# Optimization experiments

Hardware: AMD Instinct MI355X
Metric: run time of the kernel (lower is better)

## Reference

```python
import math
import jax, jax.numpy as jnp
import numpy as np

B, N, D = 4, 4096, 1024
H, DH = 16, 64  # D == H * DH


def setup_inputs() -> dict:
    key = jax.random.key(0)
    ks = jax.random.split(key, 7)
    s = 1.0 / math.sqrt(D)
    return {
        "tens": jax.random.normal(ks[0], (B, N, D), dtype=jnp.float32),
        "Wq": jax.random.normal(ks[1], (D, D), dtype=jnp.float32) * s,
        "bq": jax.random.normal(ks[2], (D,), dtype=jnp.float32) * 0.01,
        "Wk": jax.random.normal(ks[3], (D, D), dtype=jnp.float32) * s,
        "bk": jax.random.normal(ks[4], (D,), dtype=jnp.float32) * 0.01,
        "Wv": jax.random.normal(ks[5], (D, D), dtype=jnp.float32) * s,
        "bv": jax.random.normal(ks[6], (D,), dtype=jnp.float32) * 0.01,
    }


def reference(tens, Wq, bq, Wk, bk, Wv, bv):
    b, n, d = tens.shape
    # projections (torch Linear: x @ W^T + b)
    q = (tens @ Wq.T + bq).reshape(b, n, H, DH)  # [B,N,H,DH]
    k = (tens @ Wk.T + bk).reshape(b, n, H, DH)
    v = (tens @ Wv.T + bv).reshape(b, n, H, DH)
    scale = (1.0 / math.sqrt(DH)) / math.sqrt(n)
    # No softmax between QK^T and V => linear, reassociate as Q @ (K^T V)
    # to avoid the O(N^2) attention matrix; identical math.
    ktv = jnp.einsum("bnhd,bnhe->bhde", k, v)          # [B,H,DH,DH]
    out = jnp.einsum("bnhd,bhde->bnhe", q, ktv) * scale  # [B,N,H,DH]
    return out.reshape(b, n, d)
```

## Files before the change

### kernel.cpp

```cpp
#include <hip/hip_runtime.h>

typedef unsigned short ushort_t;
typedef __attribute__((ext_vector_type(8))) __bf16 bf16x8;
typedef __attribute__((ext_vector_type(8))) unsigned short ushort8;
typedef __attribute__((ext_vector_type(4))) float floatx4;

__device__ inline unsigned short f2bf(float f) {
  union { float f; unsigned u; } x; x.f = f;
  return (unsigned short)((x.u + 0x7FFFu + ((x.u >> 16) & 1u)) >> 16);
}

__global__ void cvt_f32_bf16(const float* __restrict__ in, ushort_t* __restrict__ out, int n) {
  int i = (blockIdx.x * blockDim.x + threadIdx.x) * 8;
  if (i >= n) return;
  const float4* p = (const float4*)(in + i);
  float4 a = p[0], b = p[1];
  ushort8 o;
  o[0] = f2bf(a.x); o[1] = f2bf(a.y); o[2] = f2bf(a.z); o[3] = f2bf(a.w);
  o[4] = f2bf(b.x); o[5] = f2bf(b.y); o[6] = f2bf(b.z); o[7] = f2bf(b.w);
  *(ushort8*)(out + i) = o;
}

__device__ inline void gload_lds16(const void* g, void* l) {
  __builtin_amdgcn_global_load_lds(
      (const __attribute__((address_space(1))) unsigned int*)g,
      (__attribute__((address_space(3))) unsigned int*)l, 16, 0, 0);
}

__device__ inline void store_out(float* p, float v) { *p = v; }
__device__ inline void store_out(ushort_t* p, float v) { *p = f2bf(v); }

template <typename OutT>
__global__ void gemm_bt(const ushort_t* __restrict__ A, const ushort_t* __restrict__ Bm,
                        const float* __restrict__ bias, OutT* __restrict__ C,
                        int M, int N, long sA_, long sB_, long sBias_, long sC_) {
  const int K = 1024;

  int gx = gridDim.x, gxy = gridDim.x * gridDim.y;
  int flat = blockIdx.x + gx * blockIdx.y + gxy * blockIdx.z;
  int total = gxy * gridDim.z;
  int per = total >> 3;
  int nf = (flat & 7) * per + (flat >> 3);
  int bz = nf / gxy; int rem = nf - bz * gxy;
  int by = rem / gx; int bx = rem - by * gx;

  A += (long)bz * sA_; Bm += (long)bz * sB_; bias += (long)bz * sBias_; C += (long)bz * sC_;

  __shared__ ushort_t sA[128 * 32];
  __shared__ ushort_t sB[128 * 32];

  int t = threadIdx.x;
  int w = t >> 6, l = t & 63;
  int wy = w >> 1, wx = w & 1;
  int quad = l >> 4, m16 = l & 15;
  int mBase = by * 128, nBase = bx * 128;

  int r = l >> 2, pb = l & 3;
  int swzS = (r ^ (r >> 2)) & 3;
  int sRow0 = w * 32 + r;
  int sCol = (pb ^ swzS) * 8;
  const ushort_t* gA0 = A + (long)(mBase + sRow0) * K + sCol;
  const ushort_t* gA1 = gA0 + 16 * K;
  const ushort_t* gB0 = Bm + (long)(nBase + sRow0) * K + sCol;
  const ushort_t* gB1 = gB0 + 16 * K;
  ushort_t* lA0 = sA + (w * 2) * 512;
  ushort_t* lA1 = lA0 + 512;
  ushort_t* lB0 = sB + (w * 2) * 512;
  ushort_t* lB1 = lB0 + 512;

  int swzR = (m16 ^ (m16 >> 2)) & 3;
  int aOff = (wy * 64 + m16) * 32 + (quad ^ swzR) * 8;
  int bOff = (wx * 64 + m16) * 32 + (quad ^ swzR) * 8;

  floatx4 acc[4][4] = {};

  for (int kt = 0; kt < K; kt += 32) {
    __syncthreads();
    gload_lds16(gA0 + kt, lA0);
    gload_lds16(gA1 + kt, lA1);
    gload_lds16(gB0 + kt, lB0);
    gload_lds16(gB1 + kt, lB1);
    __syncthreads();
    bf16x8 af[4], bfr[4];
#pragma unroll
    for (int i = 0; i < 4; ++i) af[i] = *(const bf16x8*)(sA + aOff + i * 16 * 32);
#pragma unroll
    for (int i = 0; i < 4; ++i) bfr[i] = *(const bf16x8*)(sB + bOff + i * 16 * 32);
#pragma unroll
    for (int mi = 0; mi < 4; ++mi)
#pragma unroll
      for (int ni = 0; ni < 4; ++ni)
        acc[mi][ni] = __builtin_amdgcn_mfma_f32_16x16x32_bf16(af[mi], bfr[ni], acc[mi][ni], 0, 0, 0);
  }

#pragma unroll
  for (int ni = 0; ni < 4; ++ni) {
    int n = nBase + wx * 64 + ni * 16 + m16;
    float bb = bias[n];
#pragma unroll
    for (int mi = 0; mi < 4; ++mi) {
      int m0 = mBase + wy * 64 + mi * 16 + quad * 4;
      floatx4 v = acc[mi][ni];
#pragma unroll
      for (int rr = 0; rr < 4; ++rr)
        store_out(&C[(long)(m0 + rr) * N + n], v[rr] + bb);
    }
  }
}

__global__ void ktv_mfma(const ushort_t* __restrict__ Kb, const ushort_t* __restrict__ Vb,
                         float* __restrict__ part) {
  int bh = blockIdx.x, sl = blockIdx.y;
  int b = bh >> 4, h = bh & 15;
  __shared__ ushort_t sKT[64 * 40];
  __shared__ ushort_t sVT[64 * 40];
  int t = threadIdx.x;
  int w = t >> 6, l = t & 63;
  int quad = l >> 4, m16 = l & 15;
  int nr = t & 31, d0 = (t >> 5) * 8;
  long base = ((long)(b * 4096 + sl * 512)) * 1024 + h * 64;
  floatx4 acc[4] = {};
  for (int nc = 0; nc < 512; nc += 32) {
    __syncthreads();
    ushort8 kv = *(const ushort8*)(Kb + base + (long)(nc + nr) * 1024 + d0);
    ushort8 vv = *(const ushort8*)(Vb + base + (long)(nc + nr) * 1024 + d0);
#pragma unroll
    for (int i = 0; i < 8; ++i) {
      sKT[(d0 + i) * 40 + nr] = kv[i];
      sVT[(d0 + i) * 40 + nr] = vv[i];
    }
    __syncthreads();
    bf16x8 af = *(const bf16x8*)(sKT + (w * 16 + m16) * 40 + quad * 8);
#pragma unroll
    for (int j = 0; j < 4; ++j) {
      bf16x8 bf = *(const bf16x8*)(sVT + (j * 16 + m16) * 40 + quad * 8);
      acc[j] = __builtin_amdgcn_mfma_f32_16x16x32_bf16(af, bf, acc[j], 0, 0, 0);
    }
  }
  float* p = part + ((long)(bh * 8 + sl)) * 4096;
#pragma unroll
  for (int j = 0; j < 4; ++j)
#pragma unroll
    for (int rr = 0; rr < 4; ++rr)
      p[(w * 16 + quad * 4 + rr) * 64 + j * 16 + m16] = acc[j][rr];
}

__global__ void ktv_reduce(const float* __restrict__ part, float* __restrict__ ktv) {
  int i = blockIdx.x * 256 + threadIdx.x;
  int bh = i >> 12, de = i & 4095;
  float s = 0.f;
#pragma unroll
  for (int sl = 0; sl < 8; ++sl) s += part[((long)(bh * 8 + sl)) * 4096 + de];
  ktv[i] = s;
}

__global__ void make_w2(const float* __restrict__ Wq, const float* __restrict__ bq,
                        const float* __restrict__ ktv, ushort_t* __restrict__ W2T,
                        float* __restrict__ bias2, float scale) {
  int bh = blockIdx.x, cq = blockIdx.y;
  int b = bh >> 4, h = bh & 15;
  __shared__ float sKTV[64 * 64];
  __shared__ float sW[64 * 64];
  int t = threadIdx.x;
  for (int i = t * 4; i < 4096; i += 1024)
    *(float4*)(sKTV + i) = *(const float4*)(ktv + (long)bh * 4096 + i);
  __syncthreads();
  if (cq == 0 && t < 64) {
    float s = 0.f;
    for (int d = 0; d < 64; ++d) s += bq[h * 64 + d] * sKTV[d * 64 + t];
    bias2[b * 1024 + h * 64 + t] = s * scale;
  }
  int e = t >> 2, c0 = (t & 3) * 16;
  for (int ct = cq * 256; ct < cq * 256 + 256; ct += 64) {
    __syncthreads();
    {
      int d = t >> 2, cc = (t & 3) * 16;
#pragma unroll
      for (int j = 0; j < 16; j += 4)
        *(float4*)(sW + d * 64 + cc + j) =
            *(const float4*)(Wq + (long)(h * 64 + d) * 1024 + ct + cc + j);
    }
    __syncthreads();
    float outv[16] = {};
    for (int d = 0; d < 64; ++d) {
      float kv = sKTV[d * 64 + e];
#pragma unroll
      for (int j = 0; j < 16; ++j) outv[j] += sW[d * 64 + c0 + j] * kv;
    }
    ushort8 o0, o1;
#pragma unroll
    for (int j = 0; j < 8; ++j) { o0[j] = f2bf(outv[j] * scale); o1[j] = f2bf(outv[8 + j] * scale); }
    ushort_t* dst = W2T + ((long)(b * 1024 + h * 64 + e)) * 1024 + ct + c0;
    *(ushort8*)dst = o0;
    *(ushort8*)(dst + 8) = o1;
  }
}

extern "C" void kernel_launch(void* const* d_in, const int* in_sizes, int n_in,
                              void* d_out, int out_size, void* d_ws, size_t ws_size,
                              hipStream_t stream) {
  (void)in_sizes; (void)n_in; (void)out_size; (void)ws_size;
  const float* tens = (const float*)d_in[0];
  const float* Wq = (const float*)d_in[1];
  const float* bq = (const float*)d_in[2];
  const float* Wk = (const float*)d_in[3];
  const float* bk = (const float*)d_in[4];
  const float* Wv = (const float*)d_in[5];
  const float* bv = (const float*)d_in[6];
  float* out = (float*)d_out;

  char* w = (char*)d_ws;
  ushort_t* Xbf  = (ushort_t*)(w);
  ushort_t* Kbf  = (ushort_t*)(w + 33554432);
  ushort_t* Vbf  = (ushort_t*)(w + 67108864);
  ushort_t* Wkbf = (ushort_t*)(w + 100663296);
  ushort_t* Wvbf = (ushort_t*)(w + 102760448);
  float*    part = (float*)(w + 104857600);
  float*    ktv  = (float*)(w + 113246208);
  ushort_t* W2T  = (ushort_t*)(w + 114294784);
  float*    bias2= (float*)(w + 122683392);

  const float scale = (1.0f / 8.0f) / 64.0f;

  hipLaunchKernelGGL(cvt_f32_bf16, dim3(8192), dim3(256), 0, stream, tens, Xbf, 16777216);
  hipLaunchKernelGGL(cvt_f32_bf16, dim3(512), dim3(256), 0, stream, Wk, Wkbf, 1048576);
  hipLaunchKernelGGL(cvt_f32_bf16, dim3(512), dim3(256), 0, stream, Wv, Wvbf, 1048576);

  hipLaunchKernelGGL((gemm_bt<ushort_t>), dim3(8, 128, 1), dim3(256), 0, stream,
                     Xbf, Wkbf, bk, Kbf, 16384, 1024, 0L, 0L, 0L, 0L);
  hipLaunchKernelGGL((gemm_bt<ushort_t>), dim3(8, 128, 1), dim3(256), 0, stream,
                     Xbf, Wvbf, bv, Vbf, 16384, 1024, 0L, 0L, 0L, 0L);

  hipLaunchKernelGGL(ktv_mfma, dim3(64, 8), dim3(256), 0, stream, Kbf, Vbf, part);
  hipLaunchKernelGGL(ktv_reduce, dim3(1024), dim3(256), 0, stream, part, ktv);
  hipLaunchKernelGGL(make_w2, dim3(64, 4), dim3(256), 0, stream, Wq, bq, ktv, W2T, bias2, scale);

  hipLaunchKernelGGL((gemm_bt<float>), dim3(8, 32, 4), dim3(256), 0, stream,
                     Xbf, W2T, bias2, out, 4096, 1024,
                     4194304L, 1048576L, 1024L, 4194304L);
}
```

Baseline: 316.2 us.

## Replace 128x128 GEMM with 256x256 tile, 4-stage LDS pipeline

Swaps the 128x128 single-buffered GEMM for a 256x256 tile kernel with 512 threads and a 4-deep LDS ring. It prefetches two tiles ahead with direct global-to-LDS loads and uses manual vmcnt waits with one barrier per k-step. MFMA issue priority is raised via setprio. The goal is to hide global load latency and cut LDS traffic per flop. In exchange it needs 128 KB of LDS and more accumulator registers, and the grids shrink (256 blocks for the projections and final GEMM), which may underfill 256 CUs.

```diff
diff --git a/kernel.cpp b/kernel.cpp
--- a/kernel.cpp
+++ b/kernel.cpp
@@ -31,10 +31,12 @@
 __device__ inline void store_out(ushort_t* p, float v) { *p = f2bf(v); }
 
 template <typename OutT>
-__global__ void gemm_bt(const ushort_t* __restrict__ A, const ushort_t* __restrict__ Bm,
-                        const float* __restrict__ bias, OutT* __restrict__ C,
-                        int M, int N, long sA_, long sB_, long sBias_, long sC_) {
+__global__ __launch_bounds__(512, 2) void gemm256(
+    const ushort_t* __restrict__ A, const ushort_t* __restrict__ Bm,
+    const float* __restrict__ bias, OutT* __restrict__ C,
+    int N, long sA_, long sB_, long sBias_, long sC_) {
   const int K = 1024;
+  const int NT = 32;
 
   int gx = gridDim.x, gxy = gridDim.x * gridDim.y;
   int flat = blockIdx.x + gx * blockIdx.y + gxy * blockIdx.z;
@@ -46,60 +48,78 @@
 
   A += (long)bz * sA_; Bm += (long)bz * sB_; bias += (long)bz * sBias_; C += (long)bz * sC_;
 
-  __shared__ ushort_t sA[128 * 32];
-  __shared__ ushort_t sB[128 * 32];
-
-  int t = threadIdx.x;
-  int w = t >> 6, l = t & 63;
-  int wy = w >> 1, wx = w & 1;
+  __shared__ ushort_t sA[4 * 8192];
+  __shared__ ushort_t sB[4 * 8192];
+
+  int tid = threadIdx.x;
+  int w = tid >> 6, l = tid & 63;
+  int wy = w >> 2, wx = w & 3;
   int quad = l >> 4, m16 = l & 15;
-  int mBase = by * 128, nBase = bx * 128;
-
-  int r = l >> 2, pb = l & 3;
-  int swzS = (r ^ (r >> 2)) & 3;
-  int sRow0 = w * 32 + r;
-  int sCol = (pb ^ swzS) * 8;
-  const ushort_t* gA0 = A + (long)(mBase + sRow0) * K + sCol;
-  const ushort_t* gA1 = gA0 + 16 * K;
-  const ushort_t* gB0 = Bm + (long)(nBase + sRow0) * K + sCol;
-  const ushort_t* gB1 = gB0 + 16 * K;
-  ushort_t* lA0 = sA + (w * 2) * 512;
-  ushort_t* lA1 = lA0 + 512;
-  ushort_t* lB0 = sB + (w * 2) * 512;
-  ushort_t* lB1 = lB0 + 512;
-
-  int swzR = (m16 ^ (m16 >> 2)) & 3;
-  int aOff = (wy * 64 + m16) * 32 + (quad ^ swzR) * 8;
-  int bOff = (wx * 64 + m16) * 32 + (quad ^ swzR) * 8;
-
-  floatx4 acc[4][4] = {};
-
-  for (int kt = 0; kt < K; kt += 32) {
-    __syncthreads();
-    gload_lds16(gA0 + kt, lA0);
-    gload_lds16(gA1 + kt, lA1);
-    gload_lds16(gB0 + kt, lB0);
-    gload_lds16(gB1 + kt, lB1);
-    __syncthreads();
-    bf16x8 af[4], bfr[4];
-#pragma unroll
-    for (int i = 0; i < 4; ++i) af[i] = *(const bf16x8*)(sA + aOff + i * 16 * 32);
-#pragma unroll
-    for (int i = 0; i < 4; ++i) bfr[i] = *(const bf16x8*)(sB + bOff + i * 16 * 32);
-#pragma unroll
-    for (int mi = 0; mi < 4; ++mi)
-#pragma unroll
-      for (int ni = 0; ni < 4; ++ni)
-        acc[mi][ni] = __builtin_amdgcn_mfma_f32_16x16x32_bf16(af[mi], bfr[ni], acc[mi][ni], 0, 0, 0);
-  }
+  int mBase = by * 256, nBase = bx * 256;
+
+  int r0 = tid >> 2, p = tid & 3;
+  int blk = (p ^ ((r0 >> 1) & 3)) << 3;
+  const ushort_t* gA0 = A + (long)(mBase + r0) * K + blk;
+  const ushort_t* gA1 = gA0 + 128 * K;
+  const ushort_t* gB0 = Bm + (long)(nBase + r0) * K + blk;
+  const ushort_t* gB1 = gB0 + 128 * K;
+  int wb = w << 9;
+
+  int swz = (m16 >> 1) & 3;
+  int aOff = (wy * 128 + m16) * 32 + ((quad ^ swz) << 3);
+  int bOff = (wx * 64 + m16) * 32 + ((quad ^ swz) << 3);
+
+  floatx4 acc[8][4] = {};
+
+  auto STAGE = [&](int tile) {
+    int ko = tile << 5;
+    int bb = (tile & 3) << 13;
+    gload_lds16(gA0 + ko, sA + bb + wb);
+    gload_lds16(gA1 + ko, sA + bb + 4096 + wb);
+    gload_lds16(gB0 + ko, sB + bb + wb);
+    gload_lds16(gB1 + ko, sB + bb + 4096 + wb);
+  };
+
+  STAGE(0);
+  STAGE(1);
+  asm volatile("s_waitcnt vmcnt(4)" ::: "memory");
+  asm volatile("s_barrier" ::: "memory");
+
+#define BODY(T, WAIT)                                                         \
+  {                                                                           \
+    const ushort_t* sa = sA + (((T) & 3) << 13);                              \
+    const ushort_t* sb = sB + (((T) & 3) << 13);                              \
+    bf16x8 af[8], bfr[4];                                                     \
+    _Pragma("unroll") for (int mi = 0; mi < 8; ++mi)                          \
+        af[mi] = *(const bf16x8*)(sa + aOff + mi * 512);                      \
+    _Pragma("unroll") for (int ni = 0; ni < 4; ++ni)                          \
+        bfr[ni] = *(const bf16x8*)(sb + bOff + ni * 512);                     \
+    WAIT;                                                                     \
+    __builtin_amdgcn_s_setprio(1);                                            \
+    _Pragma("unroll") for (int mi = 0; mi < 8; ++mi)                          \
+        _Pragma("unroll") for (int ni = 0; ni < 4; ++ni)                      \
+            acc[mi][ni] = __builtin_amdgcn_mfma_f32_16x16x32_bf16(            \
+                af[mi], bfr[ni], acc[mi][ni], 0, 0, 0);                       \
+    __builtin_amdgcn_s_setprio(0);                                            \
+  }
+
+  for (int t = 0; t < NT - 2; ++t) {
+    STAGE(t + 2);
+    BODY(t, asm volatile("s_waitcnt vmcnt(4)" ::: "memory"));
+    asm volatile("s_barrier" ::: "memory");
+  }
+  BODY(NT - 2, asm volatile("s_waitcnt vmcnt(0)" ::: "memory"));
+  asm volatile("s_barrier" ::: "memory");
+  BODY(NT - 1, );
+#undef BODY
 
 #pragma unroll
   for (int ni = 0; ni < 4; ++ni) {
     int n = nBase + wx * 64 + ni * 16 + m16;
     float bb = bias[n];
 #pragma unroll
-    for (int mi = 0; mi < 4; ++mi) {
-      int m0 = mBase + wy * 64 + mi * 16 + quad * 4;
+    for (int mi = 0; mi < 8; ++mi) {
+      int m0 = mBase + wy * 128 + mi * 16 + quad * 4;
       floatx4 v = acc[mi][ni];
 #pragma unroll
       for (int rr = 0; rr < 4; ++rr)
@@ -137,12 +157,12 @@
       acc[j] = __builtin_amdgcn_mfma_f32_16x16x32_bf16(af, bf, acc[j], 0, 0, 0);
     }
   }
-  float* p = part + ((long)(bh * 8 + sl)) * 4096;
+  float* pp = part + ((long)(bh * 8 + sl)) * 4096;
 #pragma unroll
   for (int j = 0; j < 4; ++j)
 #pragma unroll
     for (int rr = 0; rr < 4; ++rr)
-      p[(w * 16 + quad * 4 + rr) * 64 + j * 16 + m16] = acc[j][rr];
+      pp[(w * 16 + quad * 4 + rr) * 64 + j * 16 + m16] = acc[j][rr];
 }
 
 __global__ void ktv_reduce(const float* __restrict__ part, float* __restrict__ ktv) {
@@ -226,16 +246,16 @@
   hipLaunchKernelGGL(cvt_f32_bf16, dim3(512), dim3(256), 0, stream, Wk, Wkbf, 1048576);
   hipLaunchKernelGGL(cvt_f32_bf16, dim3(512), dim3(256), 0, stream, Wv, Wvbf, 1048576);
 
-  hipLaunchKernelGGL((gemm_bt<ushort_t>), dim3(8, 128, 1), dim3(256), 0, stream,
-                     Xbf, Wkbf, bk, Kbf, 16384, 1024, 0L, 0L, 0L, 0L);
-  hipLaunchKernelGGL((gemm_bt<ushort_t>), dim3(8, 128, 1), dim3(256), 0, stream,
-                     Xbf, Wvbf, bv, Vbf, 16384, 1024, 0L, 0L, 0L, 0L);
+  hipLaunchKernelGGL((gemm256<ushort_t>), dim3(4, 64, 1), dim3(512), 0, stream,
+                     Xbf, Wkbf, bk, Kbf, 1024, 0L, 0L, 0L, 0L);
+  hipLaunchKernelGGL((gemm256<ushort_t>), dim3(4, 64, 1), dim3(512), 0, stream,
+                     Xbf, Wvbf, bv, Vbf, 1024, 0L, 0L, 0L, 0L);
 
   hipLaunchKernelGGL(ktv_mfma, dim3(64, 8), dim3(256), 0, stream, Kbf, Vbf, part);
   hipLaunchKernelGGL(ktv_reduce, dim3(1024), dim3(256), 0, stream, part, ktv);
   hipLaunchKernelGGL(make_w2, dim3(64, 4), dim3(256), 0, stream, Wq, bq, ktv, W2T, bias2, scale);
 
-  hipLaunchKernelGGL((gemm_bt<float>), dim3(8, 32, 4), dim3(256), 0, stream,
-                     Xbf, W2T, bias2, out, 4096, 1024,
+  hipLaunchKernelGGL((gemm256<float>), dim3(4, 16, 4), dim3(512), 0, stream,
+                     Xbf, W2T, bias2, out, 1024,
                      4194304L, 1048576L, 1024L, 4194304L);
 }
```

After: 333.0 us. 5.3% more time.

## Compute KᵀV via per-batch Gram matrix XᵀX instead of materializing K and V

Applied to the files above, without the earlier changes.

Replaces the two full K and V projection GEMMs and the partial KᵀV reduction with an algebraic reformulation: compute G = XᵀX per batch (via a transposed copy of X), then T1 = Wk·G, and KᵀV per head as T1·Wvᵀ plus bias corrections built from column sums of X. This removes the large intermediate K/V writes and reads and roughly halves the big GEMM FLOPs. In exchange it adds a transpose pass over X, a column-sum pass and several small kernels. It also rounds G and T1 to bf16, which may change the accuracy profile.

```diff
diff --git a/kernel.cpp b/kernel.cpp
--- a/kernel.cpp
+++ b/kernel.cpp
@@ -8,6 +8,10 @@
 __device__ inline unsigned short f2bf(float f) {
   union { float f; unsigned u; } x; x.f = f;
   return (unsigned short)((x.u + 0x7FFFu + ((x.u >> 16) & 1u)) >> 16);
+}
+__device__ inline float bf2f(unsigned short v) {
+  union { unsigned u; float f; } x; x.u = (unsigned)v << 16;
+  return x.f;
 }
 
 __global__ void cvt_f32_bf16(const float* __restrict__ in, ushort_t* __restrict__ out, int n) {
@@ -30,12 +34,10 @@
 __device__ inline void store_out(float* p, float v) { *p = v; }
 __device__ inline void store_out(ushort_t* p, float v) { *p = f2bf(v); }
 
-template <typename OutT>
+template <int K, bool BIAS, typename OutT>
 __global__ void gemm_bt(const ushort_t* __restrict__ A, const ushort_t* __restrict__ Bm,
                         const float* __restrict__ bias, OutT* __restrict__ C,
-                        int M, int N, long sA_, long sB_, long sBias_, long sC_) {
-  const int K = 1024;
-
+                        int N, long sA_, long sB_, long sBias_, long sC_) {
   int gx = gridDim.x, gxy = gridDim.x * gridDim.y;
   int flat = blockIdx.x + gx * blockIdx.y + gxy * blockIdx.z;
   int total = gxy * gridDim.z;
@@ -44,7 +46,8 @@
   int bz = nf / gxy; int rem = nf - bz * gxy;
   int by = rem / gx; int bx = rem - by * gx;
 
-  A += (long)bz * sA_; Bm += (long)bz * sB_; bias += (long)bz * sBias_; C += (long)bz * sC_;
+  A += (long)bz * sA_; Bm += (long)bz * sB_; C += (long)bz * sC_;
+  if (BIAS) bias += (long)bz * sBias_;
 
   __shared__ ushort_t sA[128 * 32];
   __shared__ ushort_t sB[128 * 32];
@@ -96,7 +99,8 @@
 #pragma unroll
   for (int ni = 0; ni < 4; ++ni) {
     int n = nBase + wx * 64 + ni * 16 + m16;
-    float bb = bias[n];
+    float bb = 0.f;
+    if (BIAS) bb = bias[n];
 #pragma unroll
     for (int mi = 0; mi < 4; ++mi) {
       int m0 = mBase + wy * 64 + mi * 16 + quad * 4;
@@ -108,50 +112,108 @@
   }
 }
 
-__global__ void ktv_mfma(const ushort_t* __restrict__ Kb, const ushort_t* __restrict__ Vb,
-                         float* __restrict__ part) {
-  int bh = blockIdx.x, sl = blockIdx.y;
-  int b = bh >> 4, h = bh & 15;
-  __shared__ ushort_t sKT[64 * 40];
-  __shared__ ushort_t sVT[64 * 40];
-  int t = threadIdx.x;
-  int w = t >> 6, l = t & 63;
+__global__ void transpose_bf(const ushort_t* __restrict__ in, ushort_t* __restrict__ out) {
+  int b = blockIdx.z;
+  int d0 = blockIdx.x * 64;
+  int n0 = blockIdx.y * 64;
+  __shared__ ushort_t sT[64 * 72];
+  int t = threadIdx.x;
+  int nl = t >> 3;
+  int dl8 = (t & 7) * 8;
+  const ushort_t* src = in + ((long)b << 22) + (long)(n0 + nl) * 1024 + d0 + dl8;
+  ushort8 v0 = *(const ushort8*)src;
+  ushort8 v1 = *(const ushort8*)(src + 32 * 1024);
+#pragma unroll
+  for (int i = 0; i < 8; ++i) {
+    sT[(dl8 + i) * 72 + nl] = v0[i];
+    sT[(dl8 + i) * 72 + nl + 32] = v1[i];
+  }
+  __syncthreads();
+  int dl = t >> 3;
+  int nl8 = (t & 7) * 8;
+  ushort8 o0 = *(const ushort8*)(sT + dl * 72 + nl8);
+  ushort8 o1 = *(const ushort8*)(sT + (dl + 32) * 72 + nl8);
+  ushort_t* dst = out + ((long)b << 22) + (long)(d0 + dl) * 4096 + n0 + nl8;
+  *(ushort8*)dst = o0;
+  *(ushort8*)(dst + 32 * 4096) = o1;
+}
+
+__global__ void colsum(const ushort_t* __restrict__ X, float* __restrict__ s) {
+  int b = blockIdx.x & 3, chunk = blockIdx.x >> 2;
+  int t = threadIdx.x;
+  int c8 = chunk * 32 + (t & 3) * 8;
+  int ng = t >> 2;
+  const ushort_t* base = X + ((long)b << 22) + c8;
+  float a[8] = {};
+  for (int n = ng; n < 4096; n += 64) {
+    ushort8 v = *(const ushort8*)(base + (long)n * 1024);
+#pragma unroll
+    for (int i = 0; i < 8; ++i) a[i] += bf2f(v[i]);
+  }
+  __shared__ float sP[64 * 32];
+#pragma unroll
+  for (int i = 0; i < 8; ++i) sP[ng * 32 + (t & 3) * 8 + i] = a[i];
+  __syncthreads();
+  if (t < 32) {
+    float acc = 0.f;
+    for (int g = 0; g < 64; ++g) acc += sP[g * 32 + t];
+    s[b * 1024 + chunk * 32 + t] = acc;
+  }
+}
+
+__global__ void uw_kernel(const ushort_t* __restrict__ Wkbf, const ushort_t* __restrict__ Wvbf,
+                          const float* __restrict__ s, float* __restrict__ u,
+                          float* __restrict__ wv_s) {
+  int id = blockIdx.x;
+  int b = id & 3, which = (id >> 2) & 1, chunk = id >> 3;
+  const ushort_t* W = which ? Wvbf : Wkbf;
+  float* o = which ? wv_s : u;
+  __shared__ float ss[1024];
+  int t = threadIdx.x;
+  *(float4*)(ss + t * 4) = *(const float4*)(s + b * 1024 + t * 4);
+  __syncthreads();
+  int r = chunk * 256 + t;
+  const ushort_t* row = W + (long)r * 1024;
+  float acc = 0.f;
+  for (int k = 0; k < 1024; k += 8) {
+    ushort8 v = *(const ushort8*)(row + k);
+#pragma unroll
+    for (int i = 0; i < 8; ++i) acc += bf2f(v[i]) * ss[k + i];
+  }
+  o[b * 1024 + r] = acc;
+}
+
+__global__ void ktv_small(const ushort_t* __restrict__ T1, const ushort_t* __restrict__ Wvbf,
+                          const float* __restrict__ u, const float* __restrict__ wv_s,
+                          const float* __restrict__ bk, const float* __restrict__ bv,
+                          float* __restrict__ ktv) {
+  int bh = blockIdx.x; int b = bh >> 4, h = bh & 15;
+  int t = threadIdx.x, w = t >> 6, l = t & 63;
   int quad = l >> 4, m16 = l & 15;
-  int nr = t & 31, d0 = (t >> 5) * 8;
-  long base = ((long)(b * 4096 + sl * 512)) * 1024 + h * 64;
+  const ushort_t* Arow = T1 + ((long)b << 20) + (long)(h * 64 + w * 16 + m16) * 1024 + quad * 8;
+  const ushort_t* Brow = Wvbf + (long)(h * 64 + m16) * 1024 + quad * 8;
   floatx4 acc[4] = {};
-  for (int nc = 0; nc < 512; nc += 32) {
-    __syncthreads();
-    ushort8 kv = *(const ushort8*)(Kb + base + (long)(nc + nr) * 1024 + d0);
-    ushort8 vv = *(const ushort8*)(Vb + base + (long)(nc + nr) * 1024 + d0);
-#pragma unroll
-    for (int i = 0; i < 8; ++i) {
-      sKT[(d0 + i) * 40 + nr] = kv[i];
-      sVT[(d0 + i) * 40 + nr] = vv[i];
-    }
-    __syncthreads();
-    bf16x8 af = *(const bf16x8*)(sKT + (w * 16 + m16) * 40 + quad * 8);
+  for (int kt = 0; kt < 1024; kt += 32) {
+    bf16x8 af = *(const bf16x8*)(Arow + kt);
 #pragma unroll
     for (int j = 0; j < 4; ++j) {
-      bf16x8 bf = *(const bf16x8*)(sVT + (j * 16 + m16) * 40 + quad * 8);
-      acc[j] = __builtin_amdgcn_mfma_f32_16x16x32_bf16(af, bf, acc[j], 0, 0, 0);
-    }
-  }
-  float* p = part + ((long)(bh * 8 + sl)) * 4096;
-#pragma unroll
-  for (int j = 0; j < 4; ++j)
-#pragma unroll
-    for (int rr = 0; rr < 4; ++rr)
-      p[(w * 16 + quad * 4 + rr) * 64 + j * 16 + m16] = acc[j][rr];
-}
-
-__global__ void ktv_reduce(const float* __restrict__ part, float* __restrict__ ktv) {
-  int i = blockIdx.x * 256 + threadIdx.x;
-  int bh = i >> 12, de = i & 4095;
-  float s = 0.f;
-#pragma unroll
-  for (int sl = 0; sl < 8; ++sl) s += part[((long)(bh * 8 + sl)) * 4096 + de];
-  ktv[i] = s;
+      bf16x8 bfv = *(const bf16x8*)(Brow + (long)j * 16 * 1024 + kt);
+      acc[j] = __builtin_amdgcn_mfma_f32_16x16x32_bf16(af, bfv, acc[j], 0, 0, 0);
+    }
+  }
+  float* p = ktv + (long)bh * 4096;
+#pragma unroll
+  for (int j = 0; j < 4; ++j) {
+    int e = j * 16 + m16;
+    float bve = bv[h * 64 + e];
+    float wse = wv_s[b * 1024 + h * 64 + e] + 4096.f * bve;
+#pragma unroll
+    for (int rr = 0; rr < 4; ++rr) {
+      int d = w * 16 + quad * 4 + rr;
+      float corr = u[b * 1024 + h * 64 + d] * bve + bk[h * 64 + d] * wse;
+      p[d * 64 + e] = acc[j][rr] + corr;
+    }
+  }
 }
 
 __global__ void make_w2(const float* __restrict__ Wq, const float* __restrict__ bq,
@@ -211,14 +273,17 @@
 
   char* w = (char*)d_ws;
   ushort_t* Xbf  = (ushort_t*)(w);
-  ushort_t* Kbf  = (ushort_t*)(w + 33554432);
-  ushort_t* Vbf  = (ushort_t*)(w + 67108864);
-  ushort_t* Wkbf = (ushort_t*)(w + 100663296);
-  ushort_t* Wvbf = (ushort_t*)(w + 102760448);
-  float*    part = (float*)(w + 104857600);
-  float*    ktv  = (float*)(w + 113246208);
-  ushort_t* W2T  = (ushort_t*)(w + 114294784);
-  float*    bias2= (float*)(w + 122683392);
+  ushort_t* XT   = (ushort_t*)(w + 33554432);
+  ushort_t* Wkbf = (ushort_t*)(w + 67108864);
+  ushort_t* Wvbf = (ushort_t*)(w + 69206016);
+  ushort_t* Gbf  = (ushort_t*)(w + 71303168);
+  ushort_t* T1   = (ushort_t*)(w + 79691776);
+  float*    s    = (float*)(w + 88080384);
+  float*    u    = (float*)(w + 88096768);
+  float*    wv_s = (float*)(w + 88113152);
+  float*    ktv  = (float*)(w + 88129536);
+  ushort_t* W2T  = (ushort_t*)(w + 89178112);
+  float*    bias2= (float*)(w + 97566720);
 
   const float scale = (1.0f / 8.0f) / 64.0f;
 
@@ -226,16 +291,25 @@
   hipLaunchKernelGGL(cvt_f32_bf16, dim3(512), dim3(256), 0, stream, Wk, Wkbf, 1048576);
   hipLaunchKernelGGL(cvt_f32_bf16, dim3(512), dim3(256), 0, stream, Wv, Wvbf, 1048576);
 
-  hipLaunchKernelGGL((gemm_bt<ushort_t>), dim3(8, 128, 1), dim3(256), 0, stream,
-                     Xbf, Wkbf, bk, Kbf, 16384, 1024, 0L, 0L, 0L, 0L);
-  hipLaunchKernelGGL((gemm_bt<ushort_t>), dim3(8, 128, 1), dim3(256), 0, stream,
-                     Xbf, Wvbf, bv, Vbf, 16384, 1024, 0L, 0L, 0L, 0L);
-
-  hipLaunchKernelGGL(ktv_mfma, dim3(64, 8), dim3(256), 0, stream, Kbf, Vbf, part);
-  hipLaunchKernelGGL(ktv_reduce, dim3(1024), dim3(256), 0, stream, part, ktv);
+  hipLaunchKernelGGL(transpose_bf, dim3(16, 64, 4), dim3(256), 0, stream, Xbf, XT);
+  hipLaunchKernelGGL(colsum, dim3(128), dim3(256), 0, stream, Xbf, s);
+
+  hipLaunchKernelGGL((gemm_bt<4096, false, ushort_t>), dim3(8, 8, 4), dim3(256), 0, stream,
+                     XT, XT, (const float*)nullptr, Gbf, 1024,
+                     4194304L, 4194304L, 0L, 1048576L);
+
+  hipLaunchKernelGGL(uw_kernel, dim3(32), dim3(256), 0, stream, Wkbf, Wvbf, s, u, wv_s);
+
+  hipLaunchKernelGGL((gemm_bt<1024, false, ushort_t>), dim3(8, 8, 4), dim3(256), 0, stream,
+                     Wkbf, Gbf, (const float*)nullptr, T1, 1024,
+                     0L, 1048576L, 0L, 1048576L);
+
+  hipLaunchKernelGGL(ktv_small, dim3(64), dim3(256), 0, stream,
+                     T1, Wvbf, u, wv_s, bk, bv, ktv);
+
   hipLaunchKernelGGL(make_w2, dim3(64, 4), dim3(256), 0, stream, Wq, bq, ktv, W2T, bias2, scale);
 
-  hipLaunchKernelGGL((gemm_bt<float>), dim3(8, 32, 4), dim3(256), 0, stream,
-                     Xbf, W2T, bias2, out, 4096, 1024,
+  hipLaunchKernelGGL((gemm_bt<1024, true, float>), dim3(8, 32, 4), dim3(256), 0, stream,
+                     Xbf, W2T, bias2, out, 1024,
                      4194304L, 1048576L, 1024L, 4194304L);
 }
```

Measured after the change: 371.3 us. 1.17x slower.
